# Performance work log

Hardware: AMD Instinct MI355X
Metric: run time of the kernel (lower is better)

The kernel has to match this reference:

```python
import jax, jax.numpy as jnp
import numpy as np

N_NODES = 100000


def _gcn_norm(edge_index, num_nodes):
    # PyG GCNConv default: add self-loops, symmetric normalization
    row, col = edge_index[0], edge_index[1]
    loop = jnp.arange(num_nodes, dtype=edge_index.dtype)
    row = jnp.concatenate([row, loop])
    col = jnp.concatenate([col, loop])
    ones = jnp.ones(col.shape[0], dtype=jnp.float32)
    deg = jax.ops.segment_sum(ones, col, num_segments=num_nodes)
    dinv = jnp.where(deg > 0, jax.lax.rsqrt(deg), 0.0)
    norm = dinv[row] * dinv[col]  # [E + N]
    return row, col, norm


def _gcn_conv(x, W, b, row, col, norm, num_nodes):
    h = x @ W                               # [N, out] linear transform first
    msg = h[row] * norm[:, None]            # gather + edge-wise scale
    out = jax.ops.segment_sum(msg, col, num_segments=num_nodes)  # scatter-add
    return out + b


def setup_inputs() -> dict:
    key = jax.random.key(0)
    k1, k2, k3, k4 = jax.random.split(key, 4)
    E = 1600000
    x = jax.random.normal(k1, (N_NODES, 128), dtype=jnp.float32)
    edge_index = jax.random.randint(k2, (2, E), 0, N_NODES, dtype=jnp.int64)
    W1 = jax.random.normal(k3, (128, 128), dtype=jnp.float32) * (1.0 / np.sqrt(128))
    b1 = jnp.zeros((128,), dtype=jnp.float32)
    W2 = jax.random.normal(k4, (128, 64), dtype=jnp.float32) * (1.0 / np.sqrt(128))
    b2 = jnp.zeros((64,), dtype=jnp.float32)
    return {"x": x, "edge_index": edge_index, "W1": W1, "b1": b1, "W2": W2, "b2": b2}


def reference(x, edge_index, W1, b1, W2, b2):
    num_nodes = x.shape[0]
    row, col, norm = _gcn_norm(edge_index, num_nodes)
    h = _gcn_conv(x, W1, b1, row, col, norm, num_nodes)
    h = jax.nn.relu(h)
    out = _gcn_conv(h, W2, b2, row, col, norm, num_nodes)
    return out
```

## Files before the change

### kernel.cpp

```cpp
#include <hip/hip_runtime.h>
#include <hip/hip_bf16.h>

typedef unsigned short u16;
typedef short bf16x8 __attribute__((ext_vector_type(8)));
typedef float f32x4 __attribute__((ext_vector_type(4)));

__device__ __forceinline__ float bflo(unsigned u) { return __uint_as_float(u << 16); }
__device__ __forceinline__ float bfhi(unsigned u) { return __uint_as_float(u & 0xffff0000u); }
__device__ __forceinline__ u16 f2bf(float f) {
    unsigned u = __float_as_uint(f);
    return (u16)((u + 0x7fffu + ((u >> 16) & 1u)) >> 16);
}

#define CHUNK 8192
#define BN 512

__global__ __launch_bounds__(256) void hist_prep_kernel(const int* __restrict__ cols,
                                                        unsigned* __restrict__ hist,
                                                        int E, int nbuckets, int nblocksA,
                                                        const float* __restrict__ W1,
                                                        const float* __restrict__ W2,
                                                        u16* __restrict__ WT1,
                                                        u16* __restrict__ WT2) {
    int blk = blockIdx.x;
    if (blk >= nblocksA) {
        int t = (blk - nblocksA) * 256 + threadIdx.x;
        if (t < 128 * 128) {
            int n = t >> 7, k = t & 127;
            WT1[n * 128 + k] = f2bf(W1[k * 128 + n]);
        } else if (t < 128 * 128 + 64 * 128) {
            int i = t - 128 * 128;
            int n = i >> 7, k = i & 127;
            WT2[n * 128 + k] = f2bf(W2[k * 64 + n]);
        }
        return;
    }
    __shared__ unsigned h[256];
    int t = threadIdx.x;
    h[t] = 0;
    __syncthreads();
    int base = blk * CHUNK;
#pragma unroll
    for (int j = 0; j < CHUNK / 256; j++) {
        int i = base + j * 256 + t;
        if (i < E) atomicAdd(&h[((unsigned)cols[i]) >> 9], 1u);
    }
    __syncthreads();
    if (t < nbuckets) hist[blk * nbuckets + t] = h[t];
}

__global__ __launch_bounds__(256) void scanA1_kernel(unsigned* __restrict__ hist,
                                                     unsigned* __restrict__ totals,
                                                     int nblocksA, int nbuckets) {
    __shared__ unsigned s[256];
    int t = threadIdx.x, b = blockIdx.x;
    unsigned val = (t < nblocksA) ? hist[t * nbuckets + b] : 0u;
    s[t] = val;
    __syncthreads();
    for (int off = 1; off < 256; off <<= 1) {
        unsigned v = (t >= off) ? s[t - off] : 0u;
        __syncthreads();
        s[t] += v;
        __syncthreads();
    }
    if (t < nblocksA) hist[t * nbuckets + b] = s[t] - val;
    if (t == 255) totals[b] = s[255];
}

__global__ __launch_bounds__(256) void scanA2_kernel(const unsigned* __restrict__ totals,
                                                     unsigned* __restrict__ bucketbase,
                                                     int nbuckets) {
    __shared__ unsigned s[256];
    int t = threadIdx.x;
    unsigned val = (t < nbuckets) ? totals[t] : 0u;
    s[t] = val;
    __syncthreads();
    for (int off = 1; off < 256; off <<= 1) {
        unsigned v = (t >= off) ? s[t - off] : 0u;
        __syncthreads();
        s[t] += v;
        __syncthreads();
    }
    unsigned ex = s[t] - val;
    if (t < nbuckets) bucketbase[t] = ex;
    if (t == nbuckets - 1) bucketbase[nbuckets] = ex + val;
}

__global__ __launch_bounds__(256) void scatterA_kernel(const int* __restrict__ rows,
                                                       const int* __restrict__ cols,
                                                       const unsigned* __restrict__ hist,
                                                       const unsigned* __restrict__ bucketbase,
                                                       uint2* __restrict__ binned,
                                                       int E, int nbuckets) {
    __shared__ uint2 sp[CHUNK];
    __shared__ unsigned lstart[256];
    __shared__ unsigned lcur[256];
    __shared__ unsigned gbase[256];
    int t = threadIdx.x, blk = blockIdx.x;
    int base = blk * CHUNK;
    int cnt = min(CHUNK, E - base);

    lcur[t] = 0;
    __syncthreads();
    for (int i = t; i < cnt; i += 256)
        atomicAdd(&lcur[((unsigned)cols[base + i]) >> 9], 1u);
    __syncthreads();
    unsigned val = lcur[t];
    lstart[t] = val;
    __syncthreads();
    for (int off = 1; off < 256; off <<= 1) {
        unsigned v = (t >= off) ? lstart[t - off] : 0u;
        __syncthreads();
        lstart[t] += v;
        __syncthreads();
    }
    unsigned ex = lstart[t] - val;
    __syncthreads();
    lstart[t] = ex;
    lcur[t] = ex;
    if (t < nbuckets) gbase[t] = bucketbase[t] + hist[blk * nbuckets + t];
    __syncthreads();
    for (int i = t; i < cnt; i += 256) {
        unsigned c = (unsigned)cols[base + i];
        unsigned r = (unsigned)rows[base + i];
        unsigned pos = atomicAdd(&lcur[c >> 9], 1u);
        sp[pos] = make_uint2(r, c);
    }
    __syncthreads();
    for (int i = t; i < cnt; i += 256) {
        uint2 u = sp[i];
        unsigned g = u.y >> 9;
        binned[gbase[g] + (unsigned)i - lstart[g]] = u;
    }
}

__global__ __launch_bounds__(256) void binB_kernel(const uint2* __restrict__ binned,
                                                   const unsigned* __restrict__ bucketbase,
                                                   int* __restrict__ rowptr,
                                                   float* __restrict__ dinv,
                                                   int* __restrict__ srcidx,
                                                   int N, int E, int nbuckets) {
    __shared__ unsigned cnt[BN + 1];
    __shared__ unsigned sc[BN + 1];
    __shared__ unsigned ps[256];
    int t = threadIdx.x, b = blockIdx.x;
    int lo = b << 9;
    int nn = min(BN, N - lo);
    unsigned s = bucketbase[b], e = bucketbase[b + 1];

    cnt[t] = 0;
    cnt[t + 256] = 0;
    if (t == 0) cnt[BN] = 0;
    __syncthreads();
    for (unsigned i = s + t; i < e; i += 256)
        atomicAdd(&cnt[binned[i].y - lo], 1u);
    __syncthreads();

    unsigned a0 = cnt[2 * t], a1 = cnt[2 * t + 1];
    ps[t] = a0 + a1;
    __syncthreads();
    unsigned val = ps[t];
    for (int off = 1; off < 256; off <<= 1) {
        unsigned v = (t >= off) ? ps[t - off] : 0u;
        __syncthreads();
        ps[t] += v;
        __syncthreads();
    }
    unsigned ex = ps[t] - val;
    sc[2 * t] = ex;
    sc[2 * t + 1] = ex + a0;
    if (t == 255) sc[BN] = ex + val;
    __syncthreads();

    for (int n = t; n < nn; n += 256) {
        unsigned rp = s + sc[n];
        rowptr[lo + n] = (int)rp;
        dinv[lo + n] = rsqrtf((float)(sc[n + 1] - sc[n]) + 1.0f);
        cnt[n] = rp;
    }
    if (b == nbuckets - 1 && t == 0) rowptr[N] = E;
    __syncthreads();

    for (unsigned i = s + t; i < e; i += 256) {
        uint2 u = binned[i];
        unsigned slot = atomicAdd(&cnt[u.y - lo], 1u);
        srcidx[slot] = (int)u.x;
    }
}

template <int NOUT, bool IN_BF16>
__global__ __launch_bounds__(256) void gemm_mfma(const void* __restrict__ Xv,
                                                 const u16* __restrict__ WT,
                                                 const float* __restrict__ dinv,
                                                 u16* __restrict__ OutH, int nrows) {
    constexpr int LDK = 136;
    __shared__ u16 sX[64 * LDK];
    __shared__ u16 sW[NOUT * LDK];

    const int t = threadIdx.x;
    const int wv = t >> 6, lane = t & 63;
    const int m = lane & 15, q = lane >> 4;
    const int row0 = blockIdx.x * 64;

    for (int idx = t; idx < NOUT * 16; idx += 256) {
        int n = idx >> 4, c = idx & 15;
        *((uint4*)&sW[n * LDK + c * 8]) = ((const uint4*)WT)[idx];
    }
    if (IN_BF16) {
        const u16* X = (const u16*)Xv;
        for (int idx = t; idx < 64 * 16; idx += 256) {
            int r = idx >> 4, c = idx & 15;
            int gr = row0 + r;
            uint4 v = make_uint4(0u, 0u, 0u, 0u);
            if (gr < nrows) v = ((const uint4*)X)[(size_t)gr * 16 + c];
            *((uint4*)&sX[r * LDK + c * 8]) = v;
        }
    } else {
        const float* X = (const float*)Xv;
        for (int idx = t; idx < 64 * 32; idx += 256) {
            int r = idx >> 5, c = idx & 31;
            int gr = row0 + r;
            float4 v = make_float4(0.f, 0.f, 0.f, 0.f);
            if (gr < nrows) v = ((const float4*)X)[(size_t)gr * 32 + c];
            uint2 o;
            o.x = (unsigned)f2bf(v.x) | ((unsigned)f2bf(v.y) << 16);
            o.y = (unsigned)f2bf(v.z) | ((unsigned)f2bf(v.w) << 16);
            *((uint2*)&sX[r * LDK + c * 4]) = o;
        }
    }
    __syncthreads();

    f32x4 acc[NOUT / 16];
#pragma unroll
    for (int i = 0; i < NOUT / 16; i++) acc[i] = (f32x4){0.f, 0.f, 0.f, 0.f};

#pragma unroll
    for (int ks = 0; ks < 4; ks++) {
        const int k0 = ks * 32 + q * 8;
        bf16x8 a = *((const bf16x8*)&sX[(wv * 16 + m) * LDK + k0]);
#pragma unroll
        for (int nt = 0; nt < NOUT / 16; nt++) {
            bf16x8 b = *((const bf16x8*)&sW[(nt * 16 + m) * LDK + k0]);
            acc[nt] = __builtin_amdgcn_mfma_f32_16x16x32_bf16(a, b, acc[nt], 0, 0, 0);
        }
    }

#pragma unroll
    for (int r = 0; r < 4; r++) {
        int gi = row0 + wv * 16 + q * 4 + r;
        if (gi < nrows) {
            float dv = dinv[gi];
#pragma unroll
            for (int nt = 0; nt < NOUT / 16; nt++) {
                OutH[(size_t)gi * NOUT + nt * 16 + m] = f2bf(acc[nt][r] * dv);
            }
        }
    }
}

__global__ __launch_bounds__(256) void agg1_gemm2(const int* __restrict__ rowptr,
                                                  const int* __restrict__ srcidx,
                                                  const u16* __restrict__ hs,
                                                  const float* __restrict__ dinv,
                                                  const float* __restrict__ bias,
                                                  const u16* __restrict__ WT2,
                                                  u16* __restrict__ h2s, int N) {
    constexpr int WPN = 16;
    constexpr int LDK = 136;
    __shared__ u16 sO[16 * LDK];
    __shared__ u16 sW[64 * LDK];

    const int t = threadIdx.x;
    const int node_l = t / WPN;
    const int fl = t % WPN;
    const int node = blockIdx.x * 16 + node_l;
    const bool valid = node < N;

    for (int idx = t; idx < 64 * 16; idx += 256) {
        int n = idx >> 4, c = idx & 15;
        *((uint4*)&sW[n * LDK + c * 8]) = ((const uint4*)WT2)[idx];
    }

    const uint4* h128 = (const uint4*)hs;
    float a[8];
#pragma unroll
    for (int j = 0; j < 8; j++) a[j] = 0.f;

    if (valid) {
        int start = rowptr[node], end = rowptr[node + 1];
        {
            uint4 v = h128[(size_t)node * WPN + fl];
            a[0] = bflo(v.x); a[1] = bfhi(v.x); a[2] = bflo(v.y); a[3] = bfhi(v.y);
            a[4] = bflo(v.z); a[5] = bfhi(v.z); a[6] = bflo(v.w); a[7] = bfhi(v.w);
        }
        int nfull = (end - start) >> 3;
        int i = start;
        int r[8], r2[8];
        if (nfull > 0) {
#pragma unroll
            for (int j = 0; j < 8; j++) r[j] = srcidx[i + j];
        }
        for (int b = 0; b < nfull; b++) {
            uint4 u[8];
#pragma unroll
            for (int j = 0; j < 8; j++) u[j] = h128[(size_t)r[j] * WPN + fl];
            if (b + 1 < nfull) {
#pragma unroll
                for (int j = 0; j < 8; j++) r2[j] = srcidx[i + 8 + j];
            }
#pragma unroll
            for (int j = 0; j < 8; j++) {
                a[0] += bflo(u[j].x); a[1] += bfhi(u[j].x);
                a[2] += bflo(u[j].y); a[3] += bfhi(u[j].y);
                a[4] += bflo(u[j].z); a[5] += bfhi(u[j].z);
                a[6] += bflo(u[j].w); a[7] += bfhi(u[j].w);
            }
#pragma unroll
            for (int j = 0; j < 8; j++) r[j] = r2[j];
            i += 8;
        }
        if (i + 4 <= end) {
            int rr[4];
#pragma unroll
            for (int j = 0; j < 4; j++) rr[j] = srcidx[i + j];
            uint4 u[4];
#pragma unroll
            for (int j = 0; j < 4; j++) u[j] = h128[(size_t)rr[j] * WPN + fl];
#pragma unroll
            for (int j = 0; j < 4; j++) {
                a[0] += bflo(u[j].x); a[1] += bfhi(u[j].x);
                a[2] += bflo(u[j].y); a[3] += bfhi(u[j].y);
                a[4] += bflo(u[j].z); a[5] += bfhi(u[j].z);
                a[6] += bflo(u[j].w); a[7] += bfhi(u[j].w);
            }
            i += 4;
        }
        for (; i < end; ++i) {
            uint4 u = h128[(size_t)srcidx[i] * WPN + fl];
            a[0] += bflo(u.x); a[1] += bfhi(u.x);
            a[2] += bflo(u.y); a[3] += bfhi(u.y);
            a[4] += bflo(u.z); a[5] += bfhi(u.z);
            a[6] += bflo(u.w); a[7] += bfhi(u.w);
        }
    }

    float dv = valid ? dinv[node] : 0.f;
    float4 bv0 = ((const float4*)bias)[2 * fl];
    float4 bv1 = ((const float4*)bias)[2 * fl + 1];
    float o[8];
    o[0] = fmaxf(dv * a[0] + bv0.x, 0.f); o[1] = fmaxf(dv * a[1] + bv0.y, 0.f);
    o[2] = fmaxf(dv * a[2] + bv0.z, 0.f); o[3] = fmaxf(dv * a[3] + bv0.w, 0.f);
    o[4] = fmaxf(dv * a[4] + bv1.x, 0.f); o[5] = fmaxf(dv * a[5] + bv1.y, 0.f);
    o[6] = fmaxf(dv * a[6] + bv1.z, 0.f); o[7] = fmaxf(dv * a[7] + bv1.w, 0.f);
    uint4 w;
    w.x = (unsigned)f2bf(o[0]) | ((unsigned)f2bf(o[1]) << 16);
    w.y = (unsigned)f2bf(o[2]) | ((unsigned)f2bf(o[3]) << 16);
    w.z = (unsigned)f2bf(o[4]) | ((unsigned)f2bf(o[5]) << 16);
    w.w = (unsigned)f2bf(o[6]) | ((unsigned)f2bf(o[7]) << 16);
    *((uint4*)&sO[node_l * LDK + fl * 8]) = w;
    __syncthreads();

    const int wv = t >> 6, lane = t & 63;
    const int m = lane & 15, q = lane >> 4;
    f32x4 acc = (f32x4){0.f, 0.f, 0.f, 0.f};
#pragma unroll
    for (int ks = 0; ks < 4; ks++) {
        const int k0 = ks * 32 + q * 8;
        bf16x8 af = *((const bf16x8*)&sO[m * LDK + k0]);
        bf16x8 bf = *((const bf16x8*)&sW[(wv * 16 + m) * LDK + k0]);
        acc = __builtin_amdgcn_mfma_f32_16x16x32_bf16(af, bf, acc, 0, 0, 0);
    }
#pragma unroll
    for (int r = 0; r < 4; r++) {
        int gi = blockIdx.x * 16 + q * 4 + r;
        if (gi < N) {
            float dvv = dinv[gi];
            h2s[(size_t)gi * 64 + wv * 16 + m] = f2bf(acc[r] * dvv);
        }
    }
}

template <int NH, bool RELU, bool OUT_BF16>
__global__ __launch_bounds__(256) void aggregate(const int* __restrict__ rowptr,
                                                 const int* __restrict__ srcidx,
                                                 const u16* __restrict__ hs,
                                                 const float* __restrict__ dinv,
                                                 const float* __restrict__ bias,
                                                 void* __restrict__ outv, int N) {
    constexpr int WPN = NH / 8;
    int tid = blockIdx.x * 256 + threadIdx.x;
    int node = tid / WPN;
    int fl = tid % WPN;
    if (node >= N) return;

    const uint4* h128 = (const uint4*)hs;
    int start = rowptr[node], end = rowptr[node + 1];

    float a[8];
    {
        uint4 v = h128[(size_t)node * WPN + fl];
        a[0] = bflo(v.x); a[1] = bfhi(v.x); a[2] = bflo(v.y); a[3] = bfhi(v.y);
        a[4] = bflo(v.z); a[5] = bfhi(v.z); a[6] = bflo(v.w); a[7] = bfhi(v.w);
    }

    int nfull = (end - start) >> 3;
    int i = start;
    int r[8], r2[8];
    if (nfull > 0) {
#pragma unroll
        for (int j = 0; j < 8; j++) r[j] = srcidx[i + j];
    }
    for (int b = 0; b < nfull; b++) {
        uint4 u[8];
#pragma unroll
        for (int j = 0; j < 8; j++) u[j] = h128[(size_t)r[j] * WPN + fl];
        if (b + 1 < nfull) {
#pragma unroll
            for (int j = 0; j < 8; j++) r2[j] = srcidx[i + 8 + j];
        }
#pragma unroll
        for (int j = 0; j < 8; j++) {
            a[0] += bflo(u[j].x); a[1] += bfhi(u[j].x);
            a[2] += bflo(u[j].y); a[3] += bfhi(u[j].y);
            a[4] += bflo(u[j].z); a[5] += bfhi(u[j].z);
            a[6] += bflo(u[j].w); a[7] += bfhi(u[j].w);
        }
#pragma unroll
        for (int j = 0; j < 8; j++) r[j] = r2[j];
        i += 8;
    }
    if (i + 4 <= end) {
        int rr[4];
#pragma unroll
        for (int j = 0; j < 4; j++) rr[j] = srcidx[i + j];
        uint4 u[4];
#pragma unroll
        for (int j = 0; j < 4; j++) u[j] = h128[(size_t)rr[j] * WPN + fl];
#pragma unroll
        for (int j = 0; j < 4; j++) {
            a[0] += bflo(u[j].x); a[1] += bfhi(u[j].x);
            a[2] += bflo(u[j].y); a[3] += bfhi(u[j].y);
            a[4] += bflo(u[j].z); a[5] += bfhi(u[j].z);
            a[6] += bflo(u[j].w); a[7] += bfhi(u[j].w);
        }
        i += 4;
    }
    for (; i < end; ++i) {
        uint4 u = h128[(size_t)srcidx[i] * WPN + fl];
        a[0] += bflo(u.x); a[1] += bfhi(u.x);
        a[2] += bflo(u.y); a[3] += bfhi(u.y);
        a[4] += bflo(u.z); a[5] += bfhi(u.z);
        a[6] += bflo(u.w); a[7] += bfhi(u.w);
    }

    float dv = dinv[node];
    float4 bv0 = ((const float4*)bias)[2 * fl];
    float4 bv1 = ((const float4*)bias)[2 * fl + 1];
    float o[8];
    o[0] = dv * a[0] + bv0.x; o[1] = dv * a[1] + bv0.y;
    o[2] = dv * a[2] + bv0.z; o[3] = dv * a[3] + bv0.w;
    o[4] = dv * a[4] + bv1.x; o[5] = dv * a[5] + bv1.y;
    o[6] = dv * a[6] + bv1.z; o[7] = dv * a[7] + bv1.w;
    if (RELU) {
#pragma unroll
        for (int j = 0; j < 8; j++) o[j] = fmaxf(o[j], 0.f);
    }
    if (OUT_BF16) {
        uint4 w;
        w.x = (unsigned)f2bf(o[0]) | ((unsigned)f2bf(o[1]) << 16);
        w.y = (unsigned)f2bf(o[2]) | ((unsigned)f2bf(o[3]) << 16);
        w.z = (unsigned)f2bf(o[4]) | ((unsigned)f2bf(o[5]) << 16);
        w.w = (unsigned)f2bf(o[6]) | ((unsigned)f2bf(o[7]) << 16);
        ((uint4*)outv)[tid] = w;
    } else {
        ((float4*)outv)[2 * tid] = make_float4(o[0], o[1], o[2], o[3]);
        ((float4*)outv)[2 * tid + 1] = make_float4(o[4], o[5], o[6], o[7]);
    }
}

extern "C" void kernel_launch(void* const* d_in, const int* in_sizes, int n_in,
                              void* d_out, int out_size, void* d_ws, size_t ws_size,
                              hipStream_t stream) {
    const float* x  = (const float*)d_in[0];
    const int*   ei = (const int*)d_in[1];
    const float* W1 = (const float*)d_in[2];
    const float* b1 = (const float*)d_in[3];
    const float* W2 = (const float*)d_in[4];
    const float* b2 = (const float*)d_in[5];

    const int N = in_sizes[0] / 128;
    const int E = in_sizes[1] / 2;
    const int* rows = ei;
    const int* cols = ei + E;

    const int nbuckets = (N + BN - 1) / BN;
    const int nblocksA = (E + CHUNK - 1) / CHUNK;

    char* ws = (char*)d_ws;
    size_t off = 0;
    auto alloc = [&](size_t bytes) -> void* {
        void* p = ws + off;
        off = (off + bytes + 1023) & ~(size_t)1023;
        return p;
    };
    unsigned* hist       = (unsigned*)alloc((size_t)nbuckets * nblocksA * 4);
    unsigned* totals     = (unsigned*)alloc(256 * 4);
    unsigned* bucketbase = (unsigned*)alloc((size_t)(nbuckets + 1) * 4);
    uint2*    binned     = (uint2*)alloc((size_t)E * 8);
    int*      rowptr     = (int*)alloc((size_t)(N + 1) * 4);
    float*    dinv       = (float*)alloc((size_t)N * 4);
    int*      srcidx     = (int*)alloc((size_t)E * 4);
    u16*      WT1        = (u16*)alloc((size_t)128 * 128 * 2);
    u16*      WT2        = (u16*)alloc((size_t)64 * 128 * 2);
    u16*      h1s        = (u16*)alloc((size_t)N * 128 * 2);
    u16*      h2s        = (u16*)alloc((size_t)N * 64 * 2);

    hist_prep_kernel<<<nblocksA + 96, 256, 0, stream>>>(cols, hist, E, nbuckets, nblocksA,
                                                        W1, W2, WT1, WT2);
    scanA1_kernel<<<nbuckets, 256, 0, stream>>>(hist, totals, nblocksA, nbuckets);
    scanA2_kernel<<<1, 256, 0, stream>>>(totals, bucketbase, nbuckets);
    scatterA_kernel<<<nblocksA, 256, 0, stream>>>(rows, cols, hist, bucketbase, binned, E, nbuckets);
    binB_kernel<<<nbuckets, 256, 0, stream>>>(binned, bucketbase, rowptr, dinv, srcidx, N, E, nbuckets);

    gemm_mfma<128, false><<<(N + 63) / 64, 256, 0, stream>>>(x, WT1, dinv, h1s, N);

    agg1_gemm2<<<(N + 15) / 16, 256, 0, stream>>>(rowptr, srcidx, h1s, dinv, b1, WT2, h2s, N);

    aggregate<64, false, false><<<(N * 8 + 255) / 256, 256, 0, stream>>>(
        rowptr, srcidx, h2s, dinv, b2, d_out, N);
}
```

Before: 276.5 us.

## Pack binned edges into 32-bit words and double agg1_gemm2 block size

The binned edge array now stores each edge as one 32-bit word: the source row in the low 23 bits and the destination's offset within its 512-node bucket in the high 9 bits. This halves the binned write and read traffic in scatterA and binB, with the bucket index kept in a separate shared byte array. Separately, agg1_gemm2 now runs 512 threads over 32 nodes per block, so each block's WT2 load is amortised over more nodes and eight waves share the MFMA tiles. The packing assumes node indices fit in 23 bits, and the larger blocks may lower occupancy.

After: 417.7 us. 51.1% more time.

```diff
diff --git a/kernel.cpp b/kernel.cpp
--- a/kernel.cpp
+++ b/kernel.cpp
@@ -2,6 +2,7 @@
 #include <hip/hip_bf16.h>
 
 typedef unsigned short u16;
+typedef unsigned char u8;
 typedef short bf16x8 __attribute__((ext_vector_type(8)));
 typedef float f32x4 __attribute__((ext_vector_type(4)));
 
@@ -14,6 +15,8 @@
 
 #define CHUNK 8192
 #define BN 512
+
+#define PK_RMASK 0x7fffffu
 
 __global__ __launch_bounds__(256) void hist_prep_kernel(const int* __restrict__ cols,
                                                         unsigned* __restrict__ hist,
@@ -90,9 +93,10 @@
                                                        const int* __restrict__ cols,
                                                        const unsigned* __restrict__ hist,
                                                        const unsigned* __restrict__ bucketbase,
-                                                       uint2* __restrict__ binned,
+                                                       unsigned* __restrict__ binned,
                                                        int E, int nbuckets) {
-    __shared__ uint2 sp[CHUNK];
+    __shared__ unsigned sp[CHUNK];
+    __shared__ u8 spg[CHUNK];
     __shared__ unsigned lstart[256];
     __shared__ unsigned lcur[256];
     __shared__ unsigned gbase[256];
@@ -123,18 +127,20 @@
     for (int i = t; i < cnt; i += 256) {
         unsigned c = (unsigned)cols[base + i];
         unsigned r = (unsigned)rows[base + i];
-        unsigned pos = atomicAdd(&lcur[c >> 9], 1u);
-        sp[pos] = make_uint2(r, c);
+        unsigned g = c >> 9;
+        unsigned pos = atomicAdd(&lcur[g], 1u);
+        sp[pos] = r | ((c & 511u) << 23);
+        spg[pos] = (u8)g;
     }
     __syncthreads();
     for (int i = t; i < cnt; i += 256) {
-        uint2 u = sp[i];
-        unsigned g = u.y >> 9;
-        binned[gbase[g] + (unsigned)i - lstart[g]] = u;
-    }
-}
-
-__global__ __launch_bounds__(256) void binB_kernel(const uint2* __restrict__ binned,
+        unsigned pk = sp[i];
+        unsigned g = spg[i];
+        binned[gbase[g] + (unsigned)i - lstart[g]] = pk;
+    }
+}
+
+__global__ __launch_bounds__(256) void binB_kernel(const unsigned* __restrict__ binned,
                                                    const unsigned* __restrict__ bucketbase,
                                                    int* __restrict__ rowptr,
                                                    float* __restrict__ dinv,
@@ -153,7 +159,7 @@
     if (t == 0) cnt[BN] = 0;
     __syncthreads();
     for (unsigned i = s + t; i < e; i += 256)
-        atomicAdd(&cnt[binned[i].y - lo], 1u);
+        atomicAdd(&cnt[binned[i] >> 23], 1u);
     __syncthreads();
 
     unsigned a0 = cnt[2 * t], a1 = cnt[2 * t + 1];
@@ -182,9 +188,9 @@
     __syncthreads();
 
     for (unsigned i = s + t; i < e; i += 256) {
-        uint2 u = binned[i];
-        unsigned slot = atomicAdd(&cnt[u.y - lo], 1u);
-        srcidx[slot] = (int)u.x;
+        unsigned pk = binned[i];
+        unsigned slot = atomicAdd(&cnt[pk >> 23], 1u);
+        srcidx[slot] = (int)(pk & PK_RMASK);
     }
 }
 
@@ -258,25 +264,26 @@
     }
 }
 
-__global__ __launch_bounds__(256) void agg1_gemm2(const int* __restrict__ rowptr,
-                                                  const int* __restrict__ srcidx,
-                                                  const u16* __restrict__ hs,
-                                                  const float* __restrict__ dinv,
-                                                  const float* __restrict__ bias,
-                                                  const u16* __restrict__ WT2,
-                                                  u16* __restrict__ h2s, int N) {
+__global__ __launch_bounds__(512, 8) void agg1_gemm2(const int* __restrict__ rowptr,
+                                                     const int* __restrict__ srcidx,
+                                                     const u16* __restrict__ hs,
+                                                     const float* __restrict__ dinv,
+                                                     const float* __restrict__ bias,
+                                                     const u16* __restrict__ WT2,
+                                                     u16* __restrict__ h2s, int N) {
     constexpr int WPN = 16;
     constexpr int LDK = 136;
-    __shared__ u16 sO[16 * LDK];
+    constexpr int NPB = 32;
+    __shared__ u16 sO[NPB * LDK];
     __shared__ u16 sW[64 * LDK];
 
     const int t = threadIdx.x;
     const int node_l = t / WPN;
     const int fl = t % WPN;
-    const int node = blockIdx.x * 16 + node_l;
+    const int node = blockIdx.x * NPB + node_l;
     const bool valid = node < N;
 
-    for (int idx = t; idx < 64 * 16; idx += 256) {
+    for (int idx = t; idx < 64 * 16; idx += 512) {
         int n = idx >> 4, c = idx & 15;
         *((uint4*)&sW[n * LDK + c * 8]) = ((const uint4*)WT2)[idx];
     }
@@ -362,20 +369,22 @@
 
     const int wv = t >> 6, lane = t & 63;
     const int m = lane & 15, q = lane >> 4;
+    const int nh = wv >> 2;
+    const int ft = wv & 3;
     f32x4 acc = (f32x4){0.f, 0.f, 0.f, 0.f};
 #pragma unroll
     for (int ks = 0; ks < 4; ks++) {
         const int k0 = ks * 32 + q * 8;
-        bf16x8 af = *((const bf16x8*)&sO[m * LDK + k0]);
-        bf16x8 bf = *((const bf16x8*)&sW[(wv * 16 + m) * LDK + k0]);
+        bf16x8 af = *((const bf16x8*)&sO[(nh * 16 + m) * LDK + k0]);
+        bf16x8 bf = *((const bf16x8*)&sW[(ft * 16 + m) * LDK + k0]);
         acc = __builtin_amdgcn_mfma_f32_16x16x32_bf16(af, bf, acc, 0, 0, 0);
     }
 #pragma unroll
     for (int r = 0; r < 4; r++) {
-        int gi = blockIdx.x * 16 + q * 4 + r;
+        int gi = blockIdx.x * NPB + nh * 16 + q * 4 + r;
         if (gi < N) {
             float dvv = dinv[gi];
-            h2s[(size_t)gi * 64 + wv * 16 + m] = f2bf(acc[r] * dvv);
+            h2s[(size_t)gi * 64 + ft * 16 + m] = f2bf(acc[r] * dvv);
         }
     }
 }
@@ -506,7 +515,7 @@
     unsigned* hist       = (unsigned*)alloc((size_t)nbuckets * nblocksA * 4);
     unsigned* totals     = (unsigned*)alloc(256 * 4);
     unsigned* bucketbase = (unsigned*)alloc((size_t)(nbuckets + 1) * 4);
-    uint2*    binned     = (uint2*)alloc((size_t)E * 8);
+    unsigned* binned     = (unsigned*)alloc((size_t)E * 4);
     int*      rowptr     = (int*)alloc((size_t)(N + 1) * 4);
     float*    dinv       = (float*)alloc((size_t)N * 4);
     int*      srcidx     = (int*)alloc((size_t)E * 4);
@@ -524,7 +533,7 @@
 
     gemm_mfma<128, false><<<(N + 63) / 64, 256, 0, stream>>>(x, WT1, dinv, h1s, N);
 
-    agg1_gemm2<<<(N + 15) / 16, 256, 0, stream>>>(rowptr, srcidx, h1s, dinv, b1, WT2, h2s, N);
+    agg1_gemm2<<<(N + 31) / 32, 512, 0, stream>>>(rowptr, srcidx, h1s, dinv, b1, WT2, h2s, N);
 
     aggregate<64, false, false><<<(N * 8 + 255) / 256, 256, 0, stream>>>(
         rowptr, srcidx, h2s, dinv, b2, d_out, N);
```
